# Optimization experiments

Measured on AMD Instinct MI355X. Metric: run time of the kernel, lower is better.

## Reference

```python
import jax, jax.numpy as jnp
import numpy as np

DIM = 256; HEADS = 8; DEPTH = 2; DFF = 128
T = 64      # timesteps (transformer batch dim for s_transformer)
N = 2048    # total agents
S = 256     # number of segments (scenes)
L = 8       # agents per segment (N = S*L)
HD = DIM // HEADS
LN_EPS = 1e-5


def _ln(x, w, b):
    m = x.mean(-1, keepdims=True)
    v = x.var(-1, keepdims=True)
    return (x - m) / jnp.sqrt(v + LN_EPS) * w + b


def _mha(x, qkvw, qkvb, ow, ob):
    B, Sq, D = x.shape
    qkv = x @ qkvw.T + qkvb                      # [B,Sq,3D]
    q, k, v = jnp.split(qkv, 3, axis=-1)
    def sp(t):
        return t.reshape(B, Sq, HEADS, HD).transpose(0, 2, 1, 3)
    q, k, v = sp(q), sp(k), sp(v)
    a = jax.nn.softmax(jnp.einsum('bhqd,bhkd->bhqk', q, k) * (1.0 / (HD ** 0.5)))
    o = jnp.einsum('bhqk,bhkd->bhqd', a, v).transpose(0, 2, 1, 3).reshape(B, Sq, D)
    return o @ ow.T + ob


def _layer(x, qkvw, qkvb, ow, ob, l1w, l1b, l2w, l2b, ln1w, ln1b, ln2w, ln2b):
    # PyTorch TransformerEncoderLayer, post-norm, relu FFN
    x = _ln(x + _mha(x, qkvw, qkvb, ow, ob), ln1w, ln1b)
    h = jax.nn.relu(x @ l1w.T + l1b) @ l2w.T + l2b
    return _ln(x + h, ln2w, ln2b)


def _encoder(x, qkvw, qkvb, ow, ob, l1w, l1b, l2w, l2b, ln1w, ln1b, ln2w, ln2b):
    for i in range(DEPTH):
        x = _layer(x, qkvw[i], qkvb[i], ow[i], ob[i], l1w[i], l1b[i],
                   l2w[i], l2b[i], ln1w[i], ln1b[i], ln2w[i], ln2b[i])
    return x


def setup_inputs() -> dict:
    key = jax.random.key(0)
    ks = iter(jax.random.split(key, 64))
    def rn(shape, scale=0.05):
        return jax.random.normal(next(ks), shape, dtype=jnp.float32) * scale
    inp = {}
    inp['moveinfo'] = jax.random.normal(next(ks), (N, T, 2), dtype=jnp.float32)
    starts = jnp.arange(S, dtype=jnp.int32) * L
    inp['seq_start_end'] = jnp.stack([starts, starts + L], axis=1)  # [S,2]
    inp['w_in'] = rn((DIM, 2)); inp['b_in'] = rn((DIM,))
    for p in ('s', 't'):
        inp[p + '_qkvw'] = rn((DEPTH, 3 * DIM, DIM)); inp[p + '_qkvb'] = rn((DEPTH, 3 * DIM))
        inp[p + '_ow'] = rn((DEPTH, DIM, DIM)); inp[p + '_ob'] = rn((DEPTH, DIM))
        inp[p + '_l1w'] = rn((DEPTH, DFF, DIM)); inp[p + '_l1b'] = rn((DEPTH, DFF))
        inp[p + '_l2w'] = rn((DEPTH, DIM, DFF)); inp[p + '_l2b'] = rn((DEPTH, DIM))
        inp[p + '_ln1w'] = jnp.ones((DEPTH, DIM)); inp[p + '_ln1b'] = jnp.zeros((DEPTH, DIM))
        inp[p + '_ln2w'] = jnp.ones((DEPTH, DIM)); inp[p + '_ln2b'] = jnp.zeros((DEPTH, DIM))
    return inp


def reference(moveinfo, seq_start_end, w_in, b_in,
              s_qkvw, s_qkvb, s_ow, s_ob, s_l1w, s_l1b, s_l2w, s_l2b,
              s_ln1w, s_ln1b, s_ln2w, s_ln2b,
              t_qkvw, t_qkvb, t_ow, t_ob, t_l1w, t_l1b, t_l2w, t_l2b,
              t_ln1w, t_ln1b, t_ln2w, t_ln2b):
    # to_dim: Linear(2, dim) + exact GELU
    s_in = jax.nn.gelu(jnp.einsum('ntc,dc->ntd', moveinfo, w_in) + b_in, approximate=False)
    s_in = s_in.transpose(1, 0, 2)                       # [T, N, D]
    # gather equal-length segments: ragged loop batched as one attention call
    idx = seq_start_end[:, 0][:, None] + jnp.arange(L)   # [S, L]
    seg = s_in[:, idx, :].reshape(T * S, L, DIM)         # [T*S, L, D]
    cls = jnp.full((T * S, 1, DIM), 1e-5, dtype=s_in.dtype)
    x = jnp.concatenate([cls, seg], axis=1)              # [T*S, 1+L, D]
    x = _encoder(x, s_qkvw, s_qkvb, s_ow, s_ob, s_l1w, s_l1b, s_l2w, s_l2b,
                 s_ln1w, s_ln1b, s_ln2w, s_ln2b)
    t_in = x[:, 0, :].reshape(T, S, DIM).transpose(1, 0, 2)  # [S, T, D]
    out = _encoder(t_in, t_qkvw, t_qkvb, t_ow, t_ob, t_l1w, t_l1b, t_l2w, t_l2b,
                   t_ln1w, t_ln1b, t_ln2w, t_ln2b)
    return out
```

## Files before the change

### kernel.cpp

```cpp
#include <hip/hip_runtime.h>
#include <hip/hip_bf16.h>
#include <math.h>

typedef __bf16 bf16_t;
typedef float floatx4 __attribute__((ext_vector_type(4)));
typedef bf16_t bf16x8 __attribute__((ext_vector_type(8)));

typedef __attribute__((address_space(1))) void g_void;
typedef __attribute__((address_space(3))) void lds_void;

__device__ __forceinline__ void ldg_lds16(const bf16_t* g, bf16_t* l) {
    __builtin_amdgcn_global_load_lds((g_void*)g, (lds_void*)l, 16, 0, 0);
}

__device__ __forceinline__ void unpack4(uint2 r, float* o) {
    o[0] = __uint_as_float((r.x & 0xffffu) << 16); o[1] = __uint_as_float(r.x & 0xffff0000u);
    o[2] = __uint_as_float((r.y & 0xffffu) << 16); o[3] = __uint_as_float(r.y & 0xffff0000u);
}

__global__ void cvt_weights(const float* __restrict__ sqkvw, const float* __restrict__ sow,
                            const float* __restrict__ sl1w,  const float* __restrict__ sl2w,
                            const float* __restrict__ tqkvw, const float* __restrict__ tow,
                            const float* __restrict__ tl1w,  const float* __restrict__ tl2w,
                            bf16_t* __restrict__ dst) {
    int i = blockIdx.x * 256 + threadIdx.x;
    float v;
    if      (i <  393216) v = sqkvw[i];
    else if (i <  524288) v = sow  [i -  393216];
    else if (i <  589824) v = sl1w [i -  524288];
    else if (i <  655360) v = sl2w [i -  589824];
    else if (i < 1048576) v = tqkvw[i -  655360];
    else if (i < 1179648) v = tow  [i - 1048576];
    else if (i < 1245184) v = tl1w [i - 1179648];
    else                  v = tl2w [i - 1245184];
    dst[i] = (bf16_t)v;
}

__global__ void embed_k(const float* __restrict__ mv, const float* __restrict__ w_in,
                        const float* __restrict__ b_in, bf16_t* __restrict__ x, int b0) {
    int blk = blockIdx.x; int d = threadIdx.x;
    int tok = blk % 9; int lb = blk / 9;
    size_t oidx = (size_t)blk * 256 + d;
    if (tok == 0) { x[oidx] = (bf16_t)1e-5f; return; }
    int bb = b0 + lb; int t = bb >> 8; int s = bb & 255;
    int n = s * 8 + (tok - 1);
    float m0 = mv[((size_t)n * 64 + t) * 2];
    float m1 = mv[((size_t)n * 64 + t) * 2 + 1];
    float v = m0 * w_in[2 * d] + m1 * w_in[2 * d + 1] + b_in[d];
    v = 0.5f * v * (1.0f + erff(v * 0.70710678118654752f));
    x[oidx] = (bf16_t)v;
}

__global__ void cls_k(const bf16_t* __restrict__ x, bf16_t* __restrict__ txb,
                      float* __restrict__ txf, int b0) {
    int lb = blockIdx.x; int d = threadIdx.x;
    int bb = b0 + lb; int t = bb >> 8; int s = bb & 255;
    bf16_t v = x[(size_t)lb * 2304 + d];
    size_t di = ((size_t)(s * 64 + t)) * 256 + d;
    txb[di] = v;
    txf[di] = (float)v;
}

__global__ __launch_bounds__(256) void gemm_bt(const bf16_t* __restrict__ A,
                                               const bf16_t* __restrict__ W,
                                               const float* __restrict__ bias,
                                               bf16_t* __restrict__ C,
                                               int M, int N, int K, int relu) {
    __shared__ __align__(16) bf16_t As[8192];
    __shared__ __align__(16) bf16_t Ws[8192];
    int MT = M >> 7, NT = N >> 7;
    int g = blockIdx.x;
    int m_t, n_t;
    if ((MT & 7) == 0) {
        int x = g & 7, q = g >> 3;
        m_t = (q / NT) * 8 + x;
        n_t = q % NT;
    } else {
        m_t = g / NT; n_t = g % NT;
    }
    int tid = threadIdx.x;
    int lane = tid & 63;
    int wave = tid >> 6;
    int m0 = m_t * 128;
    int n0 = n_t * 128;
    int wm = (wave & 1) * 64;
    int wn = (wave >> 1) * 64;
    int arow = tid >> 2;
    int acol = (tid & 3) * 8;
    int fm = lane & 15;
    int fq = lane >> 4;

    floatx4 acc[4][4] = {};

    const bf16_t* Ag = A + (size_t)(m0 + arow) * K + acol;
    const bf16_t* Wg = W + (size_t)(n0 + arow) * K + acol;

    for (int k0 = 0; k0 < K; k0 += 64) {
        __syncthreads();
        ldg_lds16(Ag + k0,                       &As[tid * 8]);
        ldg_lds16(Ag + k0 + (size_t)64 * K,      &As[2048 + tid * 8]);
        ldg_lds16(Ag + k0 + 32,                  &As[4096 + tid * 8]);
        ldg_lds16(Ag + k0 + 32 + (size_t)64 * K, &As[6144 + tid * 8]);
        ldg_lds16(Wg + k0,                       &Ws[tid * 8]);
        ldg_lds16(Wg + k0 + (size_t)64 * K,      &Ws[2048 + tid * 8]);
        ldg_lds16(Wg + k0 + 32,                  &Ws[4096 + tid * 8]);
        ldg_lds16(Wg + k0 + 32 + (size_t)64 * K, &Ws[6144 + tid * 8]);
        __syncthreads();

#pragma unroll
        for (int sl = 0; sl < 2; sl++) {
            int base = sl * 4096;
            bf16x8 af[4], wf[4];
#pragma unroll
            for (int mi = 0; mi < 4; mi++)
                af[mi] = *(const bf16x8*)&As[base + (wm + mi * 16 + fm) * 32 + fq * 8];
#pragma unroll
            for (int ni = 0; ni < 4; ni++)
                wf[ni] = *(const bf16x8*)&Ws[base + (wn + ni * 16 + fm) * 32 + fq * 8];
#pragma unroll
            for (int mi = 0; mi < 4; mi++)
#pragma unroll
                for (int ni = 0; ni < 4; ni++)
                    acc[mi][ni] = __builtin_amdgcn_mfma_f32_16x16x32_bf16(wf[ni], af[mi], acc[mi][ni], 0, 0, 0);
        }
    }

#pragma unroll
    for (int mi = 0; mi < 4; mi++) {
        int row = m0 + wm + mi * 16 + fm;
#pragma unroll
        for (int ni = 0; ni < 4; ni++) {
            int colb = n0 + wn + ni * 16 + fq * 4;
            float4 b4 = *(const float4*)(bias + colb);
            float v0 = acc[mi][ni][0] + b4.x;
            float v1 = acc[mi][ni][1] + b4.y;
            float v2 = acc[mi][ni][2] + b4.z;
            float v3 = acc[mi][ni][3] + b4.w;
            if (relu) {
                v0 = fmaxf(v0, 0.f); v1 = fmaxf(v1, 0.f);
                v2 = fmaxf(v2, 0.f); v3 = fmaxf(v3, 0.f);
            }
            bf16_t t4[4] = {(bf16_t)v0, (bf16_t)v1, (bf16_t)v2, (bf16_t)v3};
            *(uint2*)(C + (size_t)row * N + colb) = *(uint2*)t4;
        }
    }
}

__device__ __forceinline__ void epi_resln64(
    floatx4 (&acc)[4][4], int m0, int wn, int fm, int fq, int wave,
    const float* __restrict__ bias, const bf16_t* __restrict__ res_bf,
    const float* __restrict__ res_f, const float* __restrict__ lnw,
    const float* __restrict__ lnb, bf16_t* __restrict__ out_bf,
    float* __restrict__ out_f, float (*rs)[64], float (*rss)[64]) {
    float s[4] = {0.f, 0.f, 0.f, 0.f}, ss[4] = {0.f, 0.f, 0.f, 0.f};
#pragma unroll
    for (int mi = 0; mi < 4; mi++) {
        size_t row = (size_t)(m0 + mi * 16 + fm);
#pragma unroll
        for (int ni = 0; ni < 4; ni++) {
            int col = wn + ni * 16 + fq * 4;
            float4 b4 = *(const float4*)(bias + col);
            float r4[4];
            if (res_f) {
                float4 t = *(const float4*)(res_f + row * 256 + col);
                r4[0] = t.x; r4[1] = t.y; r4[2] = t.z; r4[3] = t.w;
            } else {
                unpack4(*(const uint2*)(res_bf + row * 256 + col), r4);
            }
            float v0 = acc[mi][ni][0] + b4.x + r4[0];
            float v1 = acc[mi][ni][1] + b4.y + r4[1];
            float v2 = acc[mi][ni][2] + b4.z + r4[2];
            float v3 = acc[mi][ni][3] + b4.w + r4[3];
            acc[mi][ni][0] = v0; acc[mi][ni][1] = v1;
            acc[mi][ni][2] = v2; acc[mi][ni][3] = v3;
            s[mi] += v0 + v1 + v2 + v3;
            ss[mi] += v0 * v0 + v1 * v1 + v2 * v2 + v3 * v3;
        }
    }
#pragma unroll
    for (int mi = 0; mi < 4; mi++) {
        s[mi]  += __shfl_xor(s[mi], 16);  s[mi]  += __shfl_xor(s[mi], 32);
        ss[mi] += __shfl_xor(ss[mi], 16); ss[mi] += __shfl_xor(ss[mi], 32);
    }
    if (fq == 0) {
#pragma unroll
        for (int mi = 0; mi < 4; mi++) {
            rs [wave][mi * 16 + fm] = s[mi];
            rss[wave][mi * 16 + fm] = ss[mi];
        }
    }
    __syncthreads();
#pragma unroll
    for (int mi = 0; mi < 4; mi++) {
        int lrow = mi * 16 + fm;
        size_t row = (size_t)(m0 + lrow);
        float mean = (rs[0][lrow] + rs[1][lrow] + rs[2][lrow] + rs[3][lrow]) * (1.f / 256.f);
        float var  = (rss[0][lrow] + rss[1][lrow] + rss[2][lrow] + rss[3][lrow]) * (1.f / 256.f)
                   - mean * mean;
        float inv = rsqrtf(var + 1e-5f);
#pragma unroll
        for (int ni = 0; ni < 4; ni++) {
            int col = wn + ni * 16 + fq * 4;
            float4 w4 = *(const float4*)(lnw + col);
            float4 bl = *(const float4*)(lnb + col);
            float o0 = (acc[mi][ni][0] - mean) * inv * w4.x + bl.x;
            float o1 = (acc[mi][ni][1] - mean) * inv * w4.y + bl.y;
            float o2 = (acc[mi][ni][2] - mean) * inv * w4.z + bl.z;
            float o3 = (acc[mi][ni][3] - mean) * inv * w4.w + bl.w;
            if (out_bf) {
                bf16_t t4[4] = {(bf16_t)o0, (bf16_t)o1, (bf16_t)o2, (bf16_t)o3};
                *(uint2*)(out_bf + row * 256 + col) = *(uint2*)t4;
            }
            if (out_f) {
                float4 t; t.x = o0; t.y = o1; t.z = o2; t.w = o3;
                *(float4*)(out_f + row * 256 + col) = t;
            }
        }
    }
}

__global__ __launch_bounds__(256) void gemm_proj_ln(const bf16_t* __restrict__ A,
                                                    const bf16_t* __restrict__ W,
                                                    const float* __restrict__ bias,
                                                    const bf16_t* __restrict__ res_bf,
                                                    const float* __restrict__ res_f,
                                                    const float* __restrict__ lnw,
                                                    const float* __restrict__ lnb,
                                                    bf16_t* __restrict__ out_bf,
                                                    float* __restrict__ out_f) {
    __shared__ __align__(16) bf16_t As[4096];
    __shared__ __align__(16) bf16_t Ws[16384];
    __shared__ float rs[4][64], rss[4][64];
    int tid = threadIdx.x;
    int lane = tid & 63, wave = tid >> 6;
    int m0 = blockIdx.x * 64;
    int wn = wave * 64;
    int arow = tid >> 2, acol = (tid & 3) * 8;
    int fm = lane & 15, fq = lane >> 4;
    floatx4 acc[4][4] = {};
    const bf16_t* Ag = A + (size_t)(m0 + arow) * 256 + acol;
    const bf16_t* Wg = W + (size_t)arow * 256 + acol;
    for (int k0 = 0; k0 < 256; k0 += 64) {
        __syncthreads();
        ldg_lds16(Ag + k0,      &As[tid * 8]);
        ldg_lds16(Ag + k0 + 32, &As[2048 + tid * 8]);
#pragma unroll
        for (int j = 0; j < 4; j++) {
            ldg_lds16(Wg + j * 16384 + k0,      &Ws[j * 2048 + tid * 8]);
            ldg_lds16(Wg + j * 16384 + k0 + 32, &Ws[8192 + j * 2048 + tid * 8]);
        }
        __syncthreads();
#pragma unroll
        for (int sl = 0; sl < 2; sl++) {
            bf16x8 af[4], wf[4];
#pragma unroll
            for (int mi = 0; mi < 4; mi++)
                af[mi] = *(const bf16x8*)&As[sl * 2048 + (mi * 16 + fm) * 32 + fq * 8];
#pragma unroll
            for (int ni = 0; ni < 4; ni++)
                wf[ni] = *(const bf16x8*)&Ws[sl * 8192 + (wn + ni * 16 + fm) * 32 + fq * 8];
#pragma unroll
            for (int mi = 0; mi < 4; mi++)
#pragma unroll
                for (int ni = 0; ni < 4; ni++)
                    acc[mi][ni] = __builtin_amdgcn_mfma_f32_16x16x32_bf16(wf[ni], af[mi], acc[mi][ni], 0, 0, 0);
        }
    }
    epi_resln64(acc, m0, wn, fm, fq, wave, bias, res_bf, res_f, lnw, lnb, out_bf, out_f, rs, rss);
}

__global__ __launch_bounds__(256) void gemm_ffn_ln(const bf16_t* __restrict__ X,
                                                   const bf16_t* __restrict__ w1,
                                                   const float* __restrict__ b1,
                                                   const bf16_t* __restrict__ w2,
                                                   const float* __restrict__ b2,
                                                   const float* __restrict__ lnw,
                                                   const float* __restrict__ lnb,
                                                   const float* __restrict__ res_f,
                                                   bf16_t* __restrict__ out_bf,
                                                   float* __restrict__ out_f) {
    __shared__ __align__(16) bf16_t As[4096];
    __shared__ __align__(16) bf16_t Ws[8192];
    __shared__ __align__(16) bf16_t Hs[10240];
    __shared__ float rs[4][64], rss[4][64];
    int tid = threadIdx.x, lane = tid & 63, wave = tid >> 6;
    int m0 = blockIdx.x * 64;
    int wn1 = wave * 32;
    int wn2 = wave * 64;
    int arow = tid >> 2, acol = (tid & 3) * 8;
    int fm = lane & 15, fq = lane >> 4;
    floatx4 acc[4][2] = {};
    const bf16_t* Ag = X + (size_t)(m0 + arow) * 256 + acol;
    const bf16_t* Wg = w1 + (size_t)arow * 256 + acol;
    for (int k0 = 0; k0 < 256; k0 += 64) {
        __syncthreads();
        ldg_lds16(Ag + k0,      &As[tid * 8]);
        ldg_lds16(Ag + k0 + 32, &As[2048 + tid * 8]);
#pragma unroll
        for (int j = 0; j < 2; j++) {
            ldg_lds16(Wg + j * 16384 + k0,      &Ws[j * 2048 + tid * 8]);
            ldg_lds16(Wg + j * 16384 + k0 + 32, &Ws[4096 + j * 2048 + tid * 8]);
        }
        __syncthreads();
#pragma unroll
        for (int sl = 0; sl < 2; sl++) {
            bf16x8 af[4], wf[2];
#pragma unroll
            for (int mi = 0; mi < 4; mi++)
                af[mi] = *(const bf16x8*)&As[sl * 2048 + (mi * 16 + fm) * 32 + fq * 8];
#pragma unroll
            for (int ni = 0; ni < 2; ni++)
                wf[ni] = *(const bf16x8*)&Ws[sl * 4096 + (wn1 + ni * 16 + fm) * 32 + fq * 8];
#pragma unroll
            for (int mi = 0; mi < 4; mi++)
#pragma unroll
                for (int ni = 0; ni < 2; ni++)
                    acc[mi][ni] = __builtin_amdgcn_mfma_f32_16x16x32_bf16(wf[ni], af[mi], acc[mi][ni], 0, 0, 0);
        }
    }
#pragma unroll
    for (int mi = 0; mi < 4; mi++) {
        int row = mi * 16 + fm;
#pragma unroll
        for (int ni = 0; ni < 2; ni++) {
            int c = wn1 + ni * 16 + fq * 4;
            float4 b4 = *(const float4*)(b1 + c);
            bf16_t t4[4];
            t4[0] = (bf16_t)fmaxf(acc[mi][ni][0] + b4.x, 0.f);
            t4[1] = (bf16_t)fmaxf(acc[mi][ni][1] + b4.y, 0.f);
            t4[2] = (bf16_t)fmaxf(acc[mi][ni][2] + b4.z, 0.f);
            t4[3] = (bf16_t)fmaxf(acc[mi][ni][3] + b4.w, 0.f);
            *(uint2*)&Hs[(c >> 5) * 2560 + row * 40 + (c & 31)] = *(uint2*)t4;
        }
    }
    __syncthreads();
    floatx4 acc2[4][4] = {};
#pragma unroll
    for (int ks = 0; ks < 4; ks++) {
        bf16x8 af2[4];
#pragma unroll
        for (int mi = 0; mi < 4; mi++)
            af2[mi] = *(const bf16x8*)&Hs[ks * 2560 + (mi * 16 + fm) * 40 + fq * 8];
#pragma unroll
        for (int ni = 0; ni < 4; ni++) {
            bf16x8 wf2 = *(const bf16x8*)(w2 + (size_t)(wn2 + ni * 16 + fm) * 128 + ks * 32 + fq * 8);
#pragma unroll
            for (int mi = 0; mi < 4; mi++)
                acc2[mi][ni] = __builtin_amdgcn_mfma_f32_16x16x32_bf16(wf2, af2[mi], acc2[mi][ni], 0, 0, 0);
        }
    }
    epi_resln64(acc2, m0, wn2, fm, fq, wave, b2, X, res_f, lnw, lnb, out_bf, out_f, rs, rss);
}

__global__ __launch_bounds__(256) void attn9_k(const bf16_t* __restrict__ qkv,
                                               bf16_t* __restrict__ ao) {
    __shared__ __align__(16) bf16_t sb[27648];
    int b = blockIdx.x; int tid = threadIdx.x;
    const uint4* src = (const uint4*)(qkv + (size_t)b * 27648);
    uint4* dstl = (uint4*)sb;
    for (int c = tid; c < 3456; c += 256) dstl[c] = src[c];
    __syncthreads();
    for (int p = tid; p < 288; p += 256) {
        int s = p / 72; int rem = p - s * 72; int h = rem / 9; int i = rem - h * 9;
        const bf16_t* B = sb + s * 6912;
        const bf16_t* qp = B + i * 768 + h * 32;
        float qf[32];
#pragma unroll
        for (int c = 0; c < 4; c++) {
            bf16x8 t8 = *(const bf16x8*)(qp + c * 8);
#pragma unroll
            for (int e = 0; e < 8; e++) qf[c * 8 + e] = (float)t8[e];
        }
        float sc[9]; float mx = -1e30f;
#pragma unroll
        for (int j = 0; j < 9; j++) {
            const bf16_t* kp = B + j * 768 + 256 + h * 32;
            float d = 0.f;
#pragma unroll
            for (int c = 0; c < 4; c++) {
                bf16x8 t8 = *(const bf16x8*)(kp + c * 8);
#pragma unroll
                for (int e = 0; e < 8; e++) d += qf[c * 8 + e] * (float)t8[e];
            }
            d *= 0.17677669529663687f;
            sc[j] = d; mx = fmaxf(mx, d);
        }
        float den = 0.f;
#pragma unroll
        for (int j = 0; j < 9; j++) { sc[j] = __expf(sc[j] - mx); den += sc[j]; }
        float inv = 1.0f / den;
        float of[32] = {};
#pragma unroll
        for (int j = 0; j < 9; j++) {
            const bf16_t* vp = B + j * 768 + 512 + h * 32;
            float w = sc[j];
#pragma unroll
            for (int c = 0; c < 4; c++) {
                bf16x8 t8 = *(const bf16x8*)(vp + c * 8);
#pragma unroll
                for (int e = 0; e < 8; e++) of[c * 8 + e] += w * (float)t8[e];
            }
        }
        bf16_t* dst = ao + ((size_t)(b * 4 + s) * 9 + i) * 256 + h * 32;
#pragma unroll
        for (int c = 0; c < 4; c++) {
            bf16x8 o8;
#pragma unroll
            for (int e = 0; e < 8; e++) o8[e] = (bf16_t)(of[c * 8 + e] * inv);
            *(bf16x8*)(dst + c * 8) = o8;
        }
    }
}

__global__ __launch_bounds__(256) void attn64_k(const bf16_t* __restrict__ qkv,
                                                bf16_t* __restrict__ ao) {
    __shared__ __align__(16) float kk[64 * 36];
    __shared__ __align__(16) float vv[64 * 36];
    __shared__ __align__(16) float pp[64 * 64];
    __shared__ float mloc[4 * 64];
    __shared__ float sloc[4 * 64];
    int s = blockIdx.x >> 3, h = blockIdx.x & 7;
    int t = threadIdx.x;
    int i = t & 63;
    int wq = t >> 6;

    {
        int r = t >> 2, c = t & 3;
        const bf16_t* kb = qkv + ((size_t)(s * 64 + r)) * 768 + h * 32 + 256 + c * 8;
        bf16x8 k8 = *(const bf16x8*)kb;
        bf16x8 v8 = *(const bf16x8*)(kb + 256);
        float* kd = &kk[r * 36 + c * 8];
        float* vd = &vv[r * 36 + c * 8];
#pragma unroll
        for (int e = 0; e < 8; e++) { kd[e] = (float)k8[e]; vd[e] = (float)v8[e]; }
    }
    const bf16_t* qb = qkv + ((size_t)(s * 64 + i)) * 768 + h * 32;
    float qf[32];
#pragma unroll
    for (int c = 0; c < 4; c++) {
        bf16x8 t8 = *(const bf16x8*)(qb + c * 8);
#pragma unroll
        for (int e = 0; e < 8; e++) qf[c * 8 + e] = (float)t8[e];
    }
    __syncthreads();

    float sc[16]; float mx = -1e30f;
#pragma unroll
    for (int jj = 0; jj < 16; jj++) {
        int j = wq * 16 + jj;
        const float* kr = &kk[j * 36];
        float d = 0.f;
#pragma unroll
        for (int c = 0; c < 8; c++) {
            float4 k4 = *(const float4*)(kr + c * 4);
            d += qf[c*4+0]*k4.x + qf[c*4+1]*k4.y + qf[c*4+2]*k4.z + qf[c*4+3]*k4.w;
        }
        d *= 0.17677669529663687f;
        sc[jj] = d; mx = fmaxf(mx, d);
    }
    float se = 0.f;
#pragma unroll
    for (int jj = 0; jj < 16; jj++) se += __expf(sc[jj] - mx);
    mloc[wq * 64 + i] = mx;
    sloc[wq * 64 + i] = se;
    __syncthreads();

    float m0 = mloc[i], m1 = mloc[64 + i], m2 = mloc[128 + i], m3 = mloc[192 + i];
    float gm = fmaxf(fmaxf(m0, m1), fmaxf(m2, m3));
    float D = sloc[i] * __expf(m0 - gm) + sloc[64 + i] * __expf(m1 - gm)
            + sloc[128 + i] * __expf(m2 - gm) + sloc[192 + i] * __expf(m3 - gm);

#pragma unroll
    for (int jj = 0; jj < 16; jj++)
        pp[(wq * 16 + jj) * 64 + i] = __expf(sc[jj] - gm);
    __syncthreads();

    float of[8] = {};
    for (int j = 0; j < 64; j++) {
        float w = pp[j * 64 + i];
        const float* vr = &vv[j * 36 + wq * 8];
        float4 va = *(const float4*)vr;
        float4 vb = *(const float4*)(vr + 4);
        of[0] += w * va.x; of[1] += w * va.y; of[2] += w * va.z; of[3] += w * va.w;
        of[4] += w * vb.x; of[5] += w * vb.y; of[6] += w * vb.z; of[7] += w * vb.w;
    }
    float invD = 1.0f / D;
    bf16_t o8[8];
#pragma unroll
    for (int e = 0; e < 8; e++) o8[e] = (bf16_t)(of[e] * invD);
    *(uint4*)(ao + ((size_t)(s * 64 + i)) * 256 + h * 32 + wq * 8) = *(uint4*)o8;
}

extern "C" void kernel_launch(void* const* d_in, const int* in_sizes, int n_in,
                              void* d_out, int out_size, void* d_ws, size_t ws_size,
                              hipStream_t stream) {
    const float* mv   = (const float*)d_in[0];
    const float* w_in = (const float*)d_in[2];
    const float* b_in = (const float*)d_in[3];
    const float* sp[12]; const float* tp[12];
    for (int i = 0; i < 12; i++) { sp[i] = (const float*)d_in[4 + i]; tp[i] = (const float*)d_in[16 + i]; }

    bf16_t* wbf = (bf16_t*)d_ws;
    bf16_t* txb = wbf + 1310720;
    float*  txf = (float*)(txb + 4194304);
    bf16_t* pool = (bf16_t*)(txf + 4194304);

    long long headB = 2621440LL + 8388608LL + 16777216LL;
    long long cand[5] = {16384, 8192, 4096, 2048, 1024};
    int BC = 1024;
    for (int c = 0; c < 5; c++) {
        long long poolB = cand[c] * 11520LL * 2;
        if (poolB < 33554432LL) poolB = 33554432LL;
        if ((size_t)(headB + poolB) <= ws_size) { BC = (int)cand[c]; break; }
    }

    cvt_weights<<<5120, 256, 0, stream>>>(sp[0], sp[2], sp[4], sp[6], tp[0], tp[2], tp[4], tp[6], wbf);

    const int M = BC * 9;
    const int MTb = M / 128;
    const int MT64 = M / 64;
    bf16_t* xc    = pool;
    bf16_t* qkvb_ = pool + (long long)BC * 2304;
    bf16_t* aob   = qkvb_ + (long long)BC * 6912;

    for (int b0 = 0; b0 < 16384; b0 += BC) {
        embed_k<<<dim3(M), 256, 0, stream>>>(mv, w_in, b_in, xc, b0);
        for (int l = 0; l < 2; l++) {
            const bf16_t* wq = wbf + 0      + l * 196608;
            const bf16_t* wo = wbf + 393216 + l * 65536;
            const bf16_t* w1 = wbf + 524288 + l * 32768;
            const bf16_t* w2 = wbf + 589824 + l * 32768;
            gemm_bt<<<dim3(MTb * 6), 256, 0, stream>>>(xc, wq, sp[1] + l * 768, qkvb_, M, 768, 256, 0);
            attn9_k<<<dim3(BC / 4), 256, 0, stream>>>(qkvb_, aob);
            gemm_proj_ln<<<dim3(MT64), 256, 0, stream>>>(aob, wo, sp[3] + l * 256,
                                                         xc, (const float*)nullptr,
                                                         sp[8] + l * 256, sp[9] + l * 256,
                                                         xc, (float*)nullptr);
            gemm_ffn_ln<<<dim3(MT64), 256, 0, stream>>>(xc, w1, sp[5] + l * 128,
                                                        w2, sp[7] + l * 256,
                                                        sp[10] + l * 256, sp[11] + l * 256,
                                                        (const float*)nullptr,
                                                        xc, (float*)nullptr);
        }
        cls_k<<<dim3(BC), 256, 0, stream>>>(xc, txb, txf, b0);
    }

    bf16_t* tqkv = pool;
    bf16_t* tao  = pool + 12582912;
    for (int l = 0; l < 2; l++) {
        gemm_bt<<<dim3(128 * 6), 256, 0, stream>>>(txb, wbf + 655360 + l * 196608, tp[1] + l * 768,
                                                   tqkv, 16384, 768, 256, 0);
        attn64_k<<<dim3(2048), 256, 0, stream>>>(tqkv, tao);
        gemm_proj_ln<<<dim3(256), 256, 0, stream>>>(tao, wbf + 1048576 + l * 65536, tp[3] + l * 256,
                                                    (const bf16_t*)nullptr, txf,
                                                    tp[8] + l * 256, tp[9] + l * 256,
                                                    txb, txf);
        gemm_ffn_ln<<<dim3(256), 256, 0, stream>>>(txb, wbf + 1179648 + l * 32768, tp[5] + l * 128,
                                                   wbf + 1245184 + l * 32768, tp[7] + l * 256,
                                                   tp[10] + l * 256, tp[11] + l * 256,
                                                   txf,
                                                   (l == 0) ? txb : (bf16_t*)nullptr,
                                                   (l == 0) ? txf : (float*)d_out);
    }
}
```

Baseline: 1.127 ms.

## Fuse spatial QKV projection GEMM with 9-token attention in one kernel

```diff
diff --git a/kernel.cpp b/kernel.cpp
--- a/kernel.cpp
+++ b/kernel.cpp
@@ -142,6 +142,102 @@
             }
             bf16_t t4[4] = {(bf16_t)v0, (bf16_t)v1, (bf16_t)v2, (bf16_t)v3};
             *(uint2*)(C + (size_t)row * N + colb) = *(uint2*)t4;
+        }
+    }
+}
+
+__global__ __launch_bounds__(320) void qkv_attn_k(const bf16_t* __restrict__ X,
+                                                  const bf16_t* __restrict__ W,
+                                                  const float* __restrict__ qb,
+                                                  bf16_t* __restrict__ ao,
+                                                  int Mtot) {
+    __shared__ __align__(16) bf16_t qkvh[2 * 80 * 104];
+    int tid = threadIdx.x;
+    int lane = tid & 63, wave = tid >> 6;
+    int fm = lane & 15, fq = lane >> 4;
+    int m0 = blockIdx.x * 72;
+    int row_l = wave * 16 + fm;
+    int rowg = m0 + row_l; if (rowg >= Mtot) rowg = Mtot - 1;
+    const bf16_t* Xr = X + (size_t)rowg * 256 + fq * 8;
+
+    for (int h0 = 0; h0 < 8; h0 += 2) {
+        floatx4 acc[12] = {};
+        for (int kk = 0; kk < 256; kk += 32) {
+            bf16x8 af = *(const bf16x8*)(Xr + kk);
+#pragma unroll
+            for (int ni = 0; ni < 12; ni++) {
+                int reg = ni >> 2, hh = (ni >> 1) & 1, half = ni & 1;
+                int ocol = reg * 256 + (h0 + hh) * 32 + half * 16;
+                bf16x8 wf = *(const bf16x8*)(W + (size_t)(ocol + fm) * 256 + kk + fq * 8);
+                acc[ni] = __builtin_amdgcn_mfma_f32_16x16x32_bf16(wf, af, acc[ni], 0, 0, 0);
+            }
+        }
+        if (h0) __syncthreads();
+#pragma unroll
+        for (int ni = 0; ni < 12; ni++) {
+            int reg = ni >> 2, hh = (ni >> 1) & 1, half = ni & 1;
+            int gcol = reg * 256 + (h0 + hh) * 32 + half * 16 + fq * 4;
+            float4 b4 = *(const float4*)(qb + gcol);
+            float v0 = acc[ni][0] + b4.x, v1 = acc[ni][1] + b4.y;
+            float v2 = acc[ni][2] + b4.z, v3 = acc[ni][3] + b4.w;
+            if (reg == 0) {
+                v0 *= 0.17677669529663687f; v1 *= 0.17677669529663687f;
+                v2 *= 0.17677669529663687f; v3 *= 0.17677669529663687f;
+            }
+            bf16_t t4[4] = {(bf16_t)v0, (bf16_t)v1, (bf16_t)v2, (bf16_t)v3};
+            int lcol = reg * 32 + half * 16 + fq * 4;
+            *(uint2*)&qkvh[hh * 8320 + row_l * 104 + lcol] = *(uint2*)t4;
+        }
+        __syncthreads();
+        if (tid < 144) {
+            int s = tid / 18, rem = tid % 18;
+            int hh = rem / 9, i = rem % 9;
+            const bf16_t* B = &qkvh[hh * 8320 + (s * 9 + i) * 104];
+            float qf[32];
+#pragma unroll
+            for (int c = 0; c < 4; c++) {
+                bf16x8 t8 = *(const bf16x8*)(B + c * 8);
+#pragma unroll
+                for (int e = 0; e < 8; e++) qf[c * 8 + e] = (float)t8[e];
+            }
+            float sc[9]; float mx = -1e30f;
+#pragma unroll
+            for (int j = 0; j < 9; j++) {
+                const bf16_t* kp = &qkvh[hh * 8320 + (s * 9 + j) * 104 + 32];
+                float d = 0.f;
+#pragma unroll
+                for (int c = 0; c < 4; c++) {
+                    bf16x8 t8 = *(const bf16x8*)(kp + c * 8);
+#pragma unroll
+                    for (int e = 0; e < 8; e++) d += qf[c * 8 + e] * (float)t8[e];
+                }
+                sc[j] = d; mx = fmaxf(mx, d);
+            }
+            float den = 0.f;
+#pragma unroll
+            for (int j = 0; j < 9; j++) { sc[j] = __expf(sc[j] - mx); den += sc[j]; }
+            float inv = 1.0f / den;
+            float of[32] = {};
+#pragma unroll
+            for (int j = 0; j < 9; j++) {
+                const bf16_t* vp = &qkvh[hh * 8320 + (s * 9 + j) * 104 + 64];
+                float w = sc[j];
+#pragma unroll
+                for (int c = 0; c < 4; c++) {
+                    bf16x8 t8 = *(const bf16x8*)(vp + c * 8);
+#pragma unroll
+                    for (int e = 0; e < 8; e++) of[c * 8 + e] += w * (float)t8[e];
+                }
+            }
+            int grow = m0 + s * 9 + i;
+            bf16_t* dst = ao + (size_t)grow * 256 + (h0 + hh) * 32;
+#pragma unroll
+            for (int c = 0; c < 4; c++) {
+                bf16x8 o8;
+#pragma unroll
+                for (int e = 0; e < 8; e++) o8[e] = (bf16_t)(of[c * 8 + e] * inv);
+                *(bf16x8*)(dst + c * 8) = o8;
+            }
         }
     }
 }
@@ -352,66 +448,6 @@
     epi_resln64(acc2, m0, wn2, fm, fq, wave, b2, X, res_f, lnw, lnb, out_bf, out_f, rs, rss);
 }
 
-__global__ __launch_bounds__(256) void attn9_k(const bf16_t* __restrict__ qkv,
-                                               bf16_t* __restrict__ ao) {
-    __shared__ __align__(16) bf16_t sb[27648];
-    int b = blockIdx.x; int tid = threadIdx.x;
-    const uint4* src = (const uint4*)(qkv + (size_t)b * 27648);
-    uint4* dstl = (uint4*)sb;
-    for (int c = tid; c < 3456; c += 256) dstl[c] = src[c];
-    __syncthreads();
-    for (int p = tid; p < 288; p += 256) {
-        int s = p / 72; int rem = p - s * 72; int h = rem / 9; int i = rem - h * 9;
-        const bf16_t* B = sb + s * 6912;
-        const bf16_t* qp = B + i * 768 + h * 32;
-        float qf[32];
-#pragma unroll
-        for (int c = 0; c < 4; c++) {
-            bf16x8 t8 = *(const bf16x8*)(qp + c * 8);
-#pragma unroll
-            for (int e = 0; e < 8; e++) qf[c * 8 + e] = (float)t8[e];
-        }
-        float sc[9]; float mx = -1e30f;
-#pragma unroll
-        for (int j = 0; j < 9; j++) {
-            const bf16_t* kp = B + j * 768 + 256 + h * 32;
-            float d = 0.f;
-#pragma unroll
-            for (int c = 0; c < 4; c++) {
-                bf16x8 t8 = *(const bf16x8*)(kp + c * 8);
-#pragma unroll
-                for (int e = 0; e < 8; e++) d += qf[c * 8 + e] * (float)t8[e];
-            }
-            d *= 0.17677669529663687f;
-            sc[j] = d; mx = fmaxf(mx, d);
-        }
-        float den = 0.f;
-#pragma unroll
-        for (int j = 0; j < 9; j++) { sc[j] = __expf(sc[j] - mx); den += sc[j]; }
-        float inv = 1.0f / den;
-        float of[32] = {};
-#pragma unroll
-        for (int j = 0; j < 9; j++) {
-            const bf16_t* vp = B + j * 768 + 512 + h * 32;
-            float w = sc[j];
-#pragma unroll
-            for (int c = 0; c < 4; c++) {
-                bf16x8 t8 = *(const bf16x8*)(vp + c * 8);
-#pragma unroll
-                for (int e = 0; e < 8; e++) of[c * 8 + e] += w * (float)t8[e];
-            }
-        }
-        bf16_t* dst = ao + ((size_t)(b * 4 + s) * 9 + i) * 256 + h * 32;
-#pragma unroll
-        for (int c = 0; c < 4; c++) {
-            bf16x8 o8;
-#pragma unroll
-            for (int e = 0; e < 8; e++) o8[e] = (bf16_t)(of[c * 8 + e] * inv);
-            *(bf16x8*)(dst + c * 8) = o8;
-        }
-    }
-}
-
 __global__ __launch_bounds__(256) void attn64_k(const bf16_t* __restrict__ qkv,
                                                 bf16_t* __restrict__ ao) {
     __shared__ __align__(16) float kk[64 * 36];
@@ -509,7 +545,7 @@
     long long cand[5] = {16384, 8192, 4096, 2048, 1024};
     int BC = 1024;
     for (int c = 0; c < 5; c++) {
-        long long poolB = cand[c] * 11520LL * 2;
+        long long poolB = cand[c] * 4608LL * 2;
         if (poolB < 33554432LL) poolB = 33554432LL;
         if ((size_t)(headB + poolB) <= ws_size) { BC = (int)cand[c]; break; }
     }
@@ -517,11 +553,9 @@
     cvt_weights<<<5120, 256, 0, stream>>>(sp[0], sp[2], sp[4], sp[6], tp[0], tp[2], tp[4], tp[6], wbf);
 
     const int M = BC * 9;
-    const int MTb = M / 128;
     const int MT64 = M / 64;
-    bf16_t* xc    = pool;
-    bf16_t* qkvb_ = pool + (long long)BC * 2304;
-    bf16_t* aob   = qkvb_ + (long long)BC * 6912;
+    bf16_t* xc  = pool;
+    bf16_t* aob = pool + (long long)BC * 2304;
 
     for (int b0 = 0; b0 < 16384; b0 += BC) {
         embed_k<<<dim3(M), 256, 0, stream>>>(mv, w_in, b_in, xc, b0);
@@ -530,8 +564,7 @@
             const bf16_t* wo = wbf + 393216 + l * 65536;
             const bf16_t* w1 = wbf + 524288 + l * 32768;
             const bf16_t* w2 = wbf + 589824 + l * 32768;
-            gemm_bt<<<dim3(MTb * 6), 256, 0, stream>>>(xc, wq, sp[1] + l * 768, qkvb_, M, 768, 256, 0);
-            attn9_k<<<dim3(BC / 4), 256, 0, stream>>>(qkvb_, aob);
+            qkv_attn_k<<<dim3(BC / 8), 320, 0, stream>>>(xc, wq, sp[1] + l * 768, aob, M);
             gemm_proj_ln<<<dim3(MT64), 256, 0, stream>>>(aob, wo, sp[3] + l * 256,
                                                          xc, (const float*)nullptr,
                                                          sp[8] + l * 256, sp[9] + l * 256,
```

New measurement: 1.598 ms. 41.9% more time.

## Double-buffer LDS tiles in GEMM kernels to overlap loads with MFMA

Applied to the files above, without the earlier changes.

```diff
diff --git a/kernel.cpp b/kernel.cpp
--- a/kernel.cpp
+++ b/kernel.cpp
@@ -85,45 +85,45 @@
     int n0 = n_t * 128;
     int wm = (wave & 1) * 64;
     int wn = (wave >> 1) * 64;
-    int arow = tid >> 2;
-    int acol = (tid & 3) * 8;
     int fm = lane & 15;
     int fq = lane >> 4;
 
     floatx4 acc[4][4] = {};
 
-    const bf16_t* Ag = A + (size_t)(m0 + arow) * K + acol;
-    const bf16_t* Wg = W + (size_t)(n0 + arow) * K + acol;
-
-    for (int k0 = 0; k0 < K; k0 += 64) {
+    const bf16_t* Ag = A + (size_t)(m0 + (tid >> 2)) * K + (tid & 3) * 8;
+    const bf16_t* Wg = W + (size_t)(n0 + (tid >> 2)) * K + (tid & 3) * 8;
+
+    auto STAGE = [&](int r, int b) {
+        int k = r * 32;
+        ldg_lds16(Ag + k,                   &As[b * 4096 + tid * 8]);
+        ldg_lds16(Ag + k + (size_t)64 * K,  &As[b * 4096 + 2048 + tid * 8]);
+        ldg_lds16(Wg + k,                   &Ws[b * 4096 + tid * 8]);
+        ldg_lds16(Wg + k + (size_t)64 * K,  &Ws[b * 4096 + 2048 + tid * 8]);
+    };
+    auto COMPUTE = [&](int b) {
+        bf16x8 af[4], wf[4];
+#pragma unroll
+        for (int mi = 0; mi < 4; mi++)
+            af[mi] = *(const bf16x8*)&As[b * 4096 + (wm + mi * 16 + fm) * 32 + fq * 8];
+#pragma unroll
+        for (int ni = 0; ni < 4; ni++)
+            wf[ni] = *(const bf16x8*)&Ws[b * 4096 + (wn + ni * 16 + fm) * 32 + fq * 8];
+#pragma unroll
+        for (int mi = 0; mi < 4; mi++)
+#pragma unroll
+            for (int ni = 0; ni < 4; ni++)
+                acc[mi][ni] = __builtin_amdgcn_mfma_f32_16x16x32_bf16(wf[ni], af[mi], acc[mi][ni], 0, 0, 0);
+    };
+
+    int nr = K >> 5;
+    STAGE(0, 0);
+    __syncthreads();
+    for (int r = 0; r + 1 < nr; ++r) {
+        STAGE(r + 1, (r + 1) & 1);
+        COMPUTE(r & 1);
         __syncthreads();
-        ldg_lds16(Ag + k0,                       &As[tid * 8]);
-        ldg_lds16(Ag + k0 + (size_t)64 * K,      &As[2048 + tid * 8]);
-        ldg_lds16(Ag + k0 + 32,                  &As[4096 + tid * 8]);
-        ldg_lds16(Ag + k0 + 32 + (size_t)64 * K, &As[6144 + tid * 8]);
-        ldg_lds16(Wg + k0,                       &Ws[tid * 8]);
-        ldg_lds16(Wg + k0 + (size_t)64 * K,      &Ws[2048 + tid * 8]);
-        ldg_lds16(Wg + k0 + 32,                  &Ws[4096 + tid * 8]);
-        ldg_lds16(Wg + k0 + 32 + (size_t)64 * K, &Ws[6144 + tid * 8]);
-        __syncthreads();
-
-#pragma unroll
-        for (int sl = 0; sl < 2; sl++) {
-            int base = sl * 4096;
-            bf16x8 af[4], wf[4];
-#pragma unroll
-            for (int mi = 0; mi < 4; mi++)
-                af[mi] = *(const bf16x8*)&As[base + (wm + mi * 16 + fm) * 32 + fq * 8];
-#pragma unroll
-            for (int ni = 0; ni < 4; ni++)
-                wf[ni] = *(const bf16x8*)&Ws[base + (wn + ni * 16 + fm) * 32 + fq * 8];
-#pragma unroll
-            for (int mi = 0; mi < 4; mi++)
-#pragma unroll
-                for (int ni = 0; ni < 4; ni++)
-                    acc[mi][ni] = __builtin_amdgcn_mfma_f32_16x16x32_bf16(wf[ni], af[mi], acc[mi][ni], 0, 0, 0);
-        }
-    }
+    }
+    COMPUTE((nr - 1) & 1);
 
 #pragma unroll
     for (int mi = 0; mi < 4; mi++) {
@@ -235,37 +235,41 @@
     int lane = tid & 63, wave = tid >> 6;
     int m0 = blockIdx.x * 64;
     int wn = wave * 64;
-    int arow = tid >> 2, acol = (tid & 3) * 8;
     int fm = lane & 15, fq = lane >> 4;
     floatx4 acc[4][4] = {};
-    const bf16_t* Ag = A + (size_t)(m0 + arow) * 256 + acol;
-    const bf16_t* Wg = W + (size_t)arow * 256 + acol;
-    for (int k0 = 0; k0 < 256; k0 += 64) {
+    const bf16_t* Ag = A + (size_t)(m0 + (tid >> 2)) * 256 + (tid & 3) * 8;
+    const bf16_t* Wg = W + (size_t)(tid >> 2) * 256 + (tid & 3) * 8;
+
+    auto STAGE = [&](int r, int b) {
+        int k = r * 32;
+        ldg_lds16(Ag + k, &As[b * 2048 + tid * 8]);
+#pragma unroll
+        for (int j = 0; j < 4; j++)
+            ldg_lds16(Wg + k + j * 16384, &Ws[b * 8192 + j * 2048 + tid * 8]);
+    };
+    auto COMPUTE = [&](int b) {
+        bf16x8 af[4], wf[4];
+#pragma unroll
+        for (int mi = 0; mi < 4; mi++)
+            af[mi] = *(const bf16x8*)&As[b * 2048 + (mi * 16 + fm) * 32 + fq * 8];
+#pragma unroll
+        for (int ni = 0; ni < 4; ni++)
+            wf[ni] = *(const bf16x8*)&Ws[b * 8192 + (wn + ni * 16 + fm) * 32 + fq * 8];
+#pragma unroll
+        for (int mi = 0; mi < 4; mi++)
+#pragma unroll
+            for (int ni = 0; ni < 4; ni++)
+                acc[mi][ni] = __builtin_amdgcn_mfma_f32_16x16x32_bf16(wf[ni], af[mi], acc[mi][ni], 0, 0, 0);
+    };
+
+    STAGE(0, 0);
+    __syncthreads();
+    for (int r = 0; r < 7; ++r) {
+        STAGE(r + 1, (r + 1) & 1);
+        COMPUTE(r & 1);
         __syncthreads();
-        ldg_lds16(Ag + k0,      &As[tid * 8]);
-        ldg_lds16(Ag + k0 + 32, &As[2048 + tid * 8]);
-#pragma unroll
-        for (int j = 0; j < 4; j++) {
-            ldg_lds16(Wg + j * 16384 + k0,      &Ws[j * 2048 + tid * 8]);
-            ldg_lds16(Wg + j * 16384 + k0 + 32, &Ws[8192 + j * 2048 + tid * 8]);
-        }
-        __syncthreads();
-#pragma unroll
-        for (int sl = 0; sl < 2; sl++) {
-            bf16x8 af[4], wf[4];
-#pragma unroll
-            for (int mi = 0; mi < 4; mi++)
-                af[mi] = *(const bf16x8*)&As[sl * 2048 + (mi * 16 + fm) * 32 + fq * 8];
-#pragma unroll
-            for (int ni = 0; ni < 4; ni++)
-                wf[ni] = *(const bf16x8*)&Ws[sl * 8192 + (wn + ni * 16 + fm) * 32 + fq * 8];
-#pragma unroll
-            for (int mi = 0; mi < 4; mi++)
-#pragma unroll
-                for (int ni = 0; ni < 4; ni++)
-                    acc[mi][ni] = __builtin_amdgcn_mfma_f32_16x16x32_bf16(wf[ni], af[mi], acc[mi][ni], 0, 0, 0);
-        }
-    }
+    }
+    COMPUTE(1);
     epi_resln64(acc, m0, wn, fm, fq, wave, bias, res_bf, res_f, lnw, lnb, out_bf, out_f, rs, rss);
 }
 
@@ -287,37 +291,42 @@
     int m0 = blockIdx.x * 64;
     int wn1 = wave * 32;
     int wn2 = wave * 64;
-    int arow = tid >> 2, acol = (tid & 3) * 8;
     int fm = lane & 15, fq = lane >> 4;
     floatx4 acc[4][2] = {};
-    const bf16_t* Ag = X + (size_t)(m0 + arow) * 256 + acol;
-    const bf16_t* Wg = w1 + (size_t)arow * 256 + acol;
-    for (int k0 = 0; k0 < 256; k0 += 64) {
+    const bf16_t* Ag = X + (size_t)(m0 + (tid >> 2)) * 256 + (tid & 3) * 8;
+    const bf16_t* Wg = w1 + (size_t)(tid >> 2) * 256 + (tid & 3) * 8;
+
+    auto STAGE = [&](int r, int b) {
+        int k = r * 32;
+        ldg_lds16(Ag + k, &As[b * 2048 + tid * 8]);
+#pragma unroll
+        for (int j = 0; j < 2; j++)
+            ldg_lds16(Wg + k + j * 16384, &Ws[b * 4096 + j * 2048 + tid * 8]);
+    };
+    auto COMPUTE = [&](int b) {
+        bf16x8 af[4], wf[2];
+#pragma unroll
+        for (int mi = 0; mi < 4; mi++)
+            af[mi] = *(const bf16x8*)&As[b * 2048 + (mi * 16 + fm) * 32 + fq * 8];
+#pragma unroll
+        for (int ni = 0; ni < 2; ni++)
+            wf[ni] = *(const bf16x8*)&Ws[b * 4096 + (wn1 + ni * 16 + fm) * 32 + fq * 8];
+#pragma unroll
+        for (int mi = 0; mi < 4; mi++)
+#pragma unroll
+            for (int ni = 0; ni < 2; ni++)
+                acc[mi][ni] = __builtin_amdgcn_mfma_f32_16x16x32_bf16(wf[ni], af[mi], acc[mi][ni], 0, 0, 0);
+    };
+
+    STAGE(0, 0);
+    __syncthreads();
+    for (int r = 0; r < 7; ++r) {
+        STAGE(r + 1, (r + 1) & 1);
+        COMPUTE(r & 1);
         __syncthreads();
-        ldg_lds16(Ag + k0,      &As[tid * 8]);
-        ldg_lds16(Ag + k0 + 32, &As[2048 + tid * 8]);
-#pragma unroll
-        for (int j = 0; j < 2; j++) {
-            ldg_lds16(Wg + j * 16384 + k0,      &Ws[j * 2048 + tid * 8]);
-            ldg_lds16(Wg + j * 16384 + k0 + 32, &Ws[4096 + j * 2048 + tid * 8]);
-        }
-        __syncthreads();
-#pragma unroll
-        for (int sl = 0; sl < 2; sl++) {
-            bf16x8 af[4], wf[2];
-#pragma unroll
-            for (int mi = 0; mi < 4; mi++)
-                af[mi] = *(const bf16x8*)&As[sl * 2048 + (mi * 16 + fm) * 32 + fq * 8];
-#pragma unroll
-            for (int ni = 0; ni < 2; ni++)
-                wf[ni] = *(const bf16x8*)&Ws[sl * 4096 + (wn1 + ni * 16 + fm) * 32 + fq * 8];
-#pragma unroll
-            for (int mi = 0; mi < 4; mi++)
-#pragma unroll
-                for (int ni = 0; ni < 2; ni++)
-                    acc[mi][ni] = __builtin_amdgcn_mfma_f32_16x16x32_bf16(wf[ni], af[mi], acc[mi][ni], 0, 0, 0);
-        }
-    }
+    }
+    COMPUTE(1);
+
 #pragma unroll
     for (int mi = 0; mi < 4; mi++) {
         int row = mi * 16 + fm;
@@ -517,7 +526,6 @@
     cvt_weights<<<5120, 256, 0, stream>>>(sp[0], sp[2], sp[4], sp[6], tp[0], tp[2], tp[4], tp[6], wbf);
 
     const int M = BC * 9;
-    const int MTb = M / 128;
     const int MT64 = M / 64;
     bf16_t* xc    = pool;
     bf16_t* qkvb_ = pool + (long long)BC * 2304;
@@ -530,7 +538,7 @@
             const bf16_t* wo = wbf + 393216 + l * 65536;
             const bf16_t* w1 = wbf + 524288 + l * 32768;
             const bf16_t* w2 = wbf + 589824 + l * 32768;
-            gemm_bt<<<dim3(MTb * 6), 256, 0, stream>>>(xc, wq, sp[1] + l * 768, qkvb_, M, 768, 256, 0);
+            gemm_bt<<<dim3((M / 128) * 6), 256, 0, stream>>>(xc, wq, sp[1] + l * 768, qkvb_, M, 768, 256, 0);
             attn9_k<<<dim3(BC / 4), 256, 0, stream>>>(qkvb_, aob);
             gemm_proj_ln<<<dim3(MT64), 256, 0, stream>>>(aob, wo, sp[3] + l * 256,
                                                          xc, (const float*)nullptr,
```

Result: no change. 1.122 ms (-0.4%).
